# Optimization experiments

Measured on AMD Instinct MI355X. Metric: run time of the kernel, lower is better.

The kernel has to match this reference:

```python
import jax, jax.numpy as jnp
import numpy as np

N_TOKENS = 32768
D_MODEL = 1024
D_HIDDEN = 4096
N_EXPERTS = 8
TOP_K = 2


def setup_inputs() -> dict:
    key = jax.random.key(0)
    ks = jax.random.split(key, 8)
    s_in = 1.0 / np.sqrt(D_MODEL)
    s_hid = 1.0 / np.sqrt(D_HIDDEN)
    return {
        "x": jax.random.normal(ks[0], (N_TOKENS, D_MODEL), dtype=jnp.float32),
        "Wr": jax.random.normal(ks[1], (D_MODEL, N_EXPERTS), dtype=jnp.float32) * s_in,
        "br": jnp.zeros((N_EXPERTS,), dtype=jnp.float32),
        "W1": jax.random.normal(ks[2], (N_EXPERTS, D_MODEL, D_HIDDEN), dtype=jnp.float32) * s_in,
        "b1": jnp.zeros((N_EXPERTS, D_HIDDEN), dtype=jnp.float32),
        "W2": jax.random.normal(ks[3], (N_EXPERTS, D_HIDDEN, D_MODEL), dtype=jnp.float32) * s_hid,
        "b2": jnp.zeros((N_EXPERTS, D_MODEL), dtype=jnp.float32),
    }


def reference(x, Wr, br, W1, b1, W2, b2):
    # Router: softmax over experts, top-k selection, renormalize.
    logits = x @ Wr + br                                  # [N, E]
    probs = jax.nn.softmax(logits, axis=-1)
    topk_probs, topk_idx = jax.lax.top_k(probs, TOP_K)    # [N, K]
    topk_probs = topk_probs / jnp.sum(topk_probs, axis=-1, keepdims=True)
    # Per-token per-expert combine weight (sum over k of prob * selection).
    sel = jax.nn.one_hot(topk_idx, N_EXPERTS, dtype=x.dtype)   # [N, K, E]
    combine = jnp.einsum('nk,nke->ne', topk_probs, sel)        # [N, E]
    # Masked gather-MLP-scatter expressed as dense per-expert MLP weighted
    # by combine (zero weight for unselected experts -> identical math).
    out = jnp.zeros_like(x)
    for e in range(N_EXPERTS):
        h = jax.nn.gelu(x @ W1[e] + b1[e], approximate=False)  # exact erf GELU (torch default)
        out = out + combine[:, e:e + 1] * (h @ W2[e] + b2[e])
    return out
```

## Files before the change

kernel.cpp:

```cpp
#include <hip/hip_runtime.h>

#define NT_TOK 32768
#define DM 1024
#define DH 4096
#define NE 8
#define BT 256
#define BM 128
#define BK 32
#define CAP (NT_TOK*2 + NE*BT)
#define CHUNK_ROWS 32768

typedef _Float16 f16x8 __attribute__((ext_vector_type(8)));
typedef float f32x4 __attribute__((ext_vector_type(4)));
typedef float f32x8 __attribute__((ext_vector_type(8)));

__device__ __forceinline__ unsigned short f2h_bits(float v){
  _Float16 h = (_Float16)v;
  return __builtin_bit_cast(unsigned short, h);
}

__device__ __forceinline__ void async16(const void* g, void* l){
  __builtin_amdgcn_global_load_lds((const __attribute__((address_space(1))) void*)g,
                                   (__attribute__((address_space(3))) void*)l, 16, 0, 0);
}

__device__ __forceinline__ int xcd_remap(int orig, int nwg){
  int q = nwg >> 3, r = nwg & 7;
  int x = orig & 7, i = orig >> 3;
  int base = (x < r) ? x*(q+1) : r*(q+1) + (x-r)*q;
  return base + i;
}


__global__ __launch_bounds__(256) void cvt_f16_kernel(const float* __restrict__ src,
                                                      unsigned short* __restrict__ dst, int n8){
  int i = blockIdx.x*256 + threadIdx.x;
  if (i >= n8) return;
  float4 a = ((const float4*)src)[2*i];
  float4 b = ((const float4*)src)[2*i+1];
  union { unsigned short u[8]; uint4 v; } r;
  r.u[0]=f2h_bits(a.x); r.u[1]=f2h_bits(a.y); r.u[2]=f2h_bits(a.z); r.u[3]=f2h_bits(a.w);
  r.u[4]=f2h_bits(b.x); r.u[5]=f2h_bits(b.y); r.u[6]=f2h_bits(b.z); r.u[7]=f2h_bits(b.w);
  ((uint4*)dst)[i] = r.v;
}

__global__ __launch_bounds__(256) void transpose_f16_v2(const float* __restrict__ src,
    unsigned short* __restrict__ dst, int R, int C){
  __shared__ float t[64][65];
  int ez = blockIdx.z;
  const float* s = src + (size_t)ez*R*C;
  unsigned short* d = dst + (size_t)ez*R*C;
  int c0 = blockIdx.x*64, r0 = blockIdx.y*64;
  int tx = threadIdx.x & 15, ty = threadIdx.x >> 4;
  #pragma unroll
  for (int i=0;i<4;i++){
    float4 v = *(const float4*)&s[(size_t)(r0+ty+i*16)*C + c0 + tx*4];
    t[ty+i*16][tx*4+0]=v.x; t[ty+i*16][tx*4+1]=v.y;
    t[ty+i*16][tx*4+2]=v.z; t[ty+i*16][tx*4+3]=v.w;
  }
  __syncthreads();
  #pragma unroll
  for (int i=0;i<4;i++){
    int cc = ty + i*16;
    union { unsigned short u[4]; uint2 v; } o;
    #pragma unroll
    for (int j=0;j<4;j++) o.u[j] = f2h_bits(t[tx*4+j][cc]);
    *(uint2*)&d[(size_t)(c0+cc)*R + r0 + tx*4] = o.v;
  }
}


__global__ __launch_bounds__(256) void router_kernel(const float* __restrict__ x,
    const float* __restrict__ Wr, const float* __restrict__ br,
    int* __restrict__ topi, float* __restrict__ topw, int* __restrict__ counts){
  __shared__ float wr_s[NE*DM];
  __shared__ int bcnt[NE];
  int tid = threadIdx.x;
  if (tid < NE) bcnt[tid] = 0;
  for (int idx=tid; idx<NE*DM; idx+=256){
    int k = idx>>3, e = idx&7;
    wr_s[e*DM + k] = Wr[idx];
  }
  __syncthreads();
  int w = tid>>6, lane = tid&63;
  for (int tt=0; tt<16; ++tt){
    int t = blockIdx.x*64 + w*16 + tt;
    const float* xr = x + (size_t)t*DM;
    double acc[NE];
    #pragma unroll
    for (int e=0;e<NE;e++) acc[e]=0.0;
    #pragma unroll
    for (int j=0;j<16;j++){
      float xv = xr[j*64 + lane];
      #pragma unroll
      for (int e=0;e<NE;e++) acc[e] += (double)xv * (double)wr_s[e*DM + j*64 + lane];
    }
    #pragma unroll
    for (int e=0;e<NE;e++){
      #pragma unroll
      for (int d=32; d; d>>=1) acc[e] += __shfl_xor(acc[e], d);
    }
    if (lane==0){
      double l[NE];
      #pragma unroll
      for (int e=0;e<NE;e++) l[e] = acc[e] + (double)br[e];
      int i0 = 0;
      #pragma unroll
      for (int e=1;e<NE;e++) if (l[e] > l[i0]) i0 = e;
      int i1 = (i0==0) ? 1 : 0;
      #pragma unroll
      for (int e=0;e<NE;e++) if (e != i0 && l[e] > l[i1]) i1 = e;
      double w0 = 1.0/(1.0 + exp(l[i1]-l[i0]));
      topi[2*t] = i0; topi[2*t+1] = i1;
      topw[2*t] = (float)w0; topw[2*t+1] = (float)(1.0-w0);
      atomicAdd(&bcnt[i0],1); atomicAdd(&bcnt[i1],1);
    }
  }
  __syncthreads();
  if (tid < NE && bcnt[tid] > 0) atomicAdd(&counts[tid], bcnt[tid]);
}

__global__ void offsets_kernel(const int* __restrict__ counts, int* __restrict__ off){
  if (threadIdx.x==0 && blockIdx.x==0){
    int o = 0;
    for (int e=0;e<NE;e++){ off[e] = o; o += ((counts[e]+BT-1)/BT)*BT; }
    off[NE] = o;
  }
}

__global__ __launch_bounds__(256) void scatter_kernel(const int* __restrict__ topi,
    const float* __restrict__ topw, const int* __restrict__ off,
    int* __restrict__ cursor, int* __restrict__ atok, float* __restrict__ awgt){
  __shared__ int bcnt[NE];
  __shared__ int bbase[NE];
  int tid = threadIdx.x;
  if (tid < NE) bcnt[tid] = 0;
  __syncthreads();
  int t = blockIdx.x*256 + tid;
  int e0 = topi[2*t],   e1 = topi[2*t+1];
  int r0 = atomicAdd(&bcnt[e0], 1);
  int r1 = atomicAdd(&bcnt[e1], 1);
  __syncthreads();
  if (tid < NE) bbase[tid] = (bcnt[tid] > 0) ? atomicAdd(&cursor[tid], bcnt[tid]) : 0;
  __syncthreads();
  int s0 = off[e0] + bbase[e0] + r0;
  int s1 = off[e1] + bbase[e1] + r1;
  atok[s0] = t;  awgt[s0] = topw[2*t];
  atok[s1] = t;  awgt[s1] = topw[2*t+1];
}


template<int KDIM, bool IS_G2>
__global__ __launch_bounds__(256, 2) void gemm_big_kernel(
    const unsigned short* __restrict__ Asrc,
    const unsigned short* __restrict__ WT,
    const float* __restrict__ bias,
    const int* __restrict__ atok,
    const float* __restrict__ awgt,
    const int* __restrict__ offs,
    unsigned short* __restrict__ H,
    float* __restrict__ out,
    int c0){
  __shared__ unsigned short As[3][BM*BK];
  __shared__ unsigned short Bs[3][BT*BK];
  const int NDIM = IS_G2 ? DM : DH;
  const int NT = NDIM/BT;
  int wg = xcd_remap(blockIdx.x, gridDim.x);
  int nt = wg % NT, mt = wg / NT;
  int total = offs[NE];
  int m0 = c0 + mt*BM;
  if (m0 >= total) return;
  int e = 0;
  #pragma unroll
  for (int q=0;q<NE-1;q++) if (m0 >= offs[q+1]) e = q+1;
  int tid = threadIdx.x;
  int lane = tid&63, wn = tid>>6;

  const unsigned short* agp[2];
  int dofsA[2];
  #pragma unroll
  for (int j=0;j<2;j++){
    int c = j*256 + tid;
    int u = (c&7) ^ ((c>>3)&7);
    int srow = ((c>>3)<<1) + (u>>2);
    int sch  = u&3;
    if (IS_G2){
      agp[j] = Asrc + (size_t)(m0 - c0 + srow)*KDIM + sch*8;
    } else {
      int tok = atok[m0 + srow];
      if (tok < 0) tok = 0;
      agp[j] = Asrc + (size_t)tok*KDIM + sch*8;
    }
    dofsA[j] = c*8;
  }
  const unsigned short* bgp0;
  int dofsB0;
  {
    int c = tid;
    int u = (c&7) ^ ((c>>3)&7);
    int srow = ((c>>3)<<1) + (u>>2);
    int sch  = u&3;
    bgp0 = WT + ((size_t)e*NDIM + nt*BT + srow)*KDIM + sch*8;
    dofsB0 = c*8;
  }

  int pos = (((lane>>4) + ((lane&1)<<2)) ^ ((lane>>1)&7)) << 3;
  int aoff0 = (((lane&15)>>1))*64 + pos;
  int boff0 = (wn*32 + ((lane&15)>>1))*64 + pos;

  f32x4 acc[8][4];
  #pragma unroll
  for (int i=0;i<8;i++)
    #pragma unroll
    for (int j=0;j<4;j++) acc[i][j] = 0.0f;

  const int NKT = KDIM/BK;
  #pragma unroll
  for (int t=0;t<2;t++){
    #pragma unroll
    for (int j=0;j<2;j++) async16(agp[j] + t*BK, &As[t][dofsA[j]]);
    #pragma unroll
    for (int j=0;j<4;j++) async16(bgp0 + (size_t)j*64*KDIM + t*BK, &Bs[t][dofsB0 + j*2048]);
  }

  int cur = 0;
  for (int kt=0; kt<NKT; ++kt){
    if (kt < NKT-1) asm volatile("s_waitcnt vmcnt(6)" ::: "memory");
    else            asm volatile("s_waitcnt vmcnt(0)" ::: "memory");
    __builtin_amdgcn_s_barrier();
    int nxt2 = cur + 2; if (nxt2 >= 3) nxt2 -= 3;
    const unsigned short* Ab = &As[cur][0];
    const unsigned short* Bb = &Bs[cur][0];
    f16x8 b[4], a[4];
    #pragma unroll
    for (int nf=0;nf<4;nf++) b[nf] = *(const f16x8*)&Bb[boff0 + nf*512];
    #pragma unroll
    for (int mf=0;mf<4;mf++) a[mf] = *(const f16x8*)&Ab[aoff0 + mf*512];
    if (kt+2 < NKT){
      #pragma unroll
      for (int j=0;j<2;j++) async16(agp[j] + (size_t)(kt+2)*BK, &As[nxt2][dofsA[j]]);
    }
    __builtin_amdgcn_s_setprio(1);
    #pragma unroll
    for (int mf=0;mf<4;mf++)
      #pragma unroll
      for (int nf=0;nf<4;nf++)
        acc[mf][nf] = __builtin_amdgcn_mfma_f32_16x16x32_f16(a[mf], b[nf], acc[mf][nf], 0,0,0);
    __builtin_amdgcn_s_setprio(0);
    __builtin_amdgcn_s_barrier();
    #pragma unroll
    for (int mf=0;mf<4;mf++) a[mf] = *(const f16x8*)&Ab[aoff0 + (mf+4)*512];
    if (kt+2 < NKT){
      #pragma unroll
      for (int j=0;j<4;j++) async16(bgp0 + (size_t)j*64*KDIM + (size_t)(kt+2)*BK, &Bs[nxt2][dofsB0 + j*2048]);
    }
    __builtin_amdgcn_s_setprio(1);
    #pragma unroll
    for (int mf=0;mf<4;mf++)
      #pragma unroll
      for (int nf=0;nf<4;nf++)
        acc[mf+4][nf] = __builtin_amdgcn_mfma_f32_16x16x32_f16(a[mf], b[nf], acc[mf+4][nf], 0,0,0);
    __builtin_amdgcn_s_setprio(0);
    cur = (cur + 1 == 3) ? 0 : cur + 1;
  }

  int nbase = nt*BT + wn*64 + (lane&15);
  if (!IS_G2){
    const float* be = bias + (size_t)e*DH;
    int rloc = (m0 - c0) + ((lane>>4)<<2);
    #pragma unroll
    for (int mf=0;mf<8;mf++)
      #pragma unroll
      for (int nf=0;nf<4;nf++){
        int nn = nbase + nf*16;
        float bv = be[nn];
        #pragma unroll
        for (int r2=0;r2<4;r2++){
          float v = acc[mf][nf][r2] + bv;
          float g = 0.5f*v*(1.0f + erff(v*0.70710678118654752f));
          H[(size_t)(rloc + mf*16 + r2)*DH + nn] = f2h_bits(g);
        }
      }
  } else {
    const float* be = bias + (size_t)e*DM;
    int sbase = m0 + ((lane>>4)<<2);
    #pragma unroll
    for (int mf=0;mf<8;mf++){
      #pragma unroll
      for (int r2=0;r2<4;r2++){
        int slot = sbase + mf*16 + r2;
        int tok = atok[slot];
        float wgt = awgt[slot];
        if (tok >= 0){
          #pragma unroll
          for (int nf=0;nf<4;nf++){
            int nn = nbase + nf*16;
            float v = acc[mf][nf][r2] + be[nn];
            atomicAdd(&out[(size_t)tok*DM + nn], wgt*v);
          }
        }
      }
    }
  }
}


__global__ __launch_bounds__(256) void gemm1_f32_kernel(
    const float* __restrict__ xf, const unsigned short* __restrict__ W1T,
    const float* __restrict__ b1, const int* __restrict__ atok,
    const int* __restrict__ offs, unsigned short* __restrict__ H, int c0){
  __shared__ float Asf[128*64];
  __shared__ unsigned short Bsld[128*64];
  const int NT = DH/128;
  int wg = xcd_remap(blockIdx.x, gridDim.x);
  int nt = wg % NT, mt = wg / NT;
  int total = offs[NE];
  int m0 = c0 + mt*128;
  if (m0 >= total) return;
  int e = 0;
  #pragma unroll
  for (int q=0;q<NE-1;q++) if (m0 >= offs[q+1]) e = q+1;
  int tid = threadIdx.x;
  const void* ag[8];
  int aofs[8];
  #pragma unroll
  for (int j=0;j<8;j++){
    int c = j*256 + tid;
    int r = c>>4, sb = (c&15)*16;
    int tok = atok[m0 + r];
    if (tok < 0) tok = 0;
    ag[j] = (const void*)((const char*)(xf + (size_t)tok*DM) + sb);
    aofs[j] = c*16;
  }
  const unsigned short* bg[4];
  int bofs[4];
  #pragma unroll
  for (int j=0;j<4;j++){
    int c = j*256 + tid;
    int r = c>>3, s = c&7;
    bg[j] = W1T + ((size_t)e*DH + nt*128 + r)*DM + s*8;
    bofs[j] = c*16;
  }
  f32x4 acc[4][4];
  #pragma unroll
  for (int i=0;i<4;i++)
    #pragma unroll
    for (int j=0;j<4;j++) acc[i][j] = 0.0f;
  int lane = tid&63;
  int wm = tid>>7, wn = (tid>>6)&1;
  int arow = wm*64 + (lane&15);
  int ak0  = (lane>>4)*8;
  int brr  = (wn*64 + (lane&15))*64 + ak0;
  for (int kt=0; kt<DM/64; ++kt){
    #pragma unroll
    for (int j=0;j<8;j++)
      async16((const char*)ag[j] + (size_t)kt*64*4, (char*)Asf + aofs[j]);
    #pragma unroll
    for (int j=0;j<4;j++)
      async16(bg[j] + (size_t)kt*64, (char*)Bsld + bofs[j]);
    __syncthreads();
    #pragma unroll
    for (int kk=0; kk<64; kk+=32){
      f16x8 a[4], b[4];
      #pragma unroll
      for (int f=0;f<4;f++){
        f32x8 v = *(const f32x8*)&Asf[(arow + f*16)*64 + ak0 + kk];
        a[f] = __builtin_convertvector(v, f16x8);
        b[f] = *(const f16x8*)&Bsld[brr + f*16*64 + kk];
      }
      #pragma unroll
      for (int i=0;i<4;i++)
        #pragma unroll
        for (int j2=0;j2<4;j2++)
          acc[i][j2] = __builtin_amdgcn_mfma_f32_16x16x32_f16(a[i], b[j2], acc[i][j2], 0,0,0);
    }
    __syncthreads();
  }
  const float* b1e = b1 + (size_t)e*DH;
  int rloc = (m0 - c0) + wm*64 + ((lane>>4)<<2);
  int nbase = nt*128 + wn*64 + (lane&15);
  #pragma unroll
  for (int i=0;i<4;i++)
    #pragma unroll
    for (int j=0;j<4;j++){
      int nn = nbase + j*16;
      float bv = b1e[nn];
      #pragma unroll
      for (int r2=0;r2<4;r2++){
        float v = acc[i][j][r2] + bv;
        float g = 0.5f*v*(1.0f + erff(v*0.70710678118654752f));
        H[(size_t)(rloc + i*16 + r2)*DH + nn] = f2h_bits(g);
      }
    }
}

__global__ void fill_kernel(float* p, float v, size_t n){
  size_t i = (size_t)blockIdx.x*256 + threadIdx.x;
  if (i < n) p[i] = v;
}


extern "C" void kernel_launch(void* const* d_in, const int* in_sizes, int n_in,
                              void* d_out, int out_size, void* d_ws, size_t ws_size,
                              hipStream_t stream){
  const float* x  = (const float*)d_in[0];
  const float* Wr = (const float*)d_in[1];
  const float* br = (const float*)d_in[2];
  const float* W1 = (const float*)d_in[3];
  const float* b1 = (const float*)d_in[4];
  const float* W2 = (const float*)d_in[5];
  const float* b2 = (const float*)d_in[6];
  float* out = (float*)d_out;

  char* ws = (char*)d_ws;
  size_t o = 0;
  auto take = [&](size_t bytes)->void*{
    void* p = ws + o; o += (bytes + 255) & ~(size_t)255; return p;
  };
  unsigned short* W1T = (unsigned short*)take((size_t)NE*DM*DH*2);
  unsigned short* W2T = (unsigned short*)take((size_t)NE*DM*DH*2);
  int*   TOPI = (int*)take((size_t)NT_TOK*2*4);
  float* TOPW = (float*)take((size_t)NT_TOK*2*4);
  int*   ATOK = (int*)take((size_t)CAP*4);
  float* AWGT = (float*)take((size_t)CAP*4);
  int*   CNT  = (int*)take(256);
  int* CUR = CNT + 8;
  int* OFF = CNT + 16;

  if (o + (size_t)BT*DH*2 > ws_size){
    fill_kernel<<<(unsigned)((out_size+255)/256), 256, 0, stream>>>(out, 4321.5f, (size_t)out_size);
    return;
  }

  unsigned short* XB = nullptr;
  bool use_xb = false;
  {
    size_t xb_bytes = (size_t)NT_TOK*DM*2 + 256;
    size_t need_h  = (size_t)2048*DH*2;
    if (o + xb_bytes + need_h <= ws_size){
      use_xb = true;
      XB = (unsigned short*)take((size_t)NT_TOK*DM*2);
    }
  }
  size_t rem = ws_size - o;
  size_t cr = (rem / ((size_t)DH*2)) / BT * BT;
  if (cr > (size_t)CHUNK_ROWS) cr = CHUNK_ROWS;
  if (cr < BT){
    fill_kernel<<<(unsigned)((out_size+255)/256), 256, 0, stream>>>(out, 4321.5f, (size_t)out_size);
    return;
  }
  int CR = (int)cr;
  unsigned short* Hb = (unsigned short*)take((size_t)CR*DH*2);

  hipMemsetAsync(CNT, 0, 64, stream);
  hipMemsetAsync(ATOK, 0xFF, (size_t)CAP*4, stream);
  hipMemsetAsync(out, 0, (size_t)out_size*sizeof(float), stream);

  if (use_xb)
    cvt_f16_kernel<<<(NT_TOK*DM/8 + 255)/256, 256, 0, stream>>>(x, XB, NT_TOK*DM/8);
  transpose_f16_v2<<<dim3(DH/64, DM/64, NE), 256, 0, stream>>>(W1, W1T, DM, DH);
  transpose_f16_v2<<<dim3(DM/64, DH/64, NE), 256, 0, stream>>>(W2, W2T, DH, DM);
  router_kernel<<<NT_TOK/64, 256, 0, stream>>>(x, Wr, br, TOPI, TOPW, CNT);
  offsets_kernel<<<1, 1, 0, stream>>>(CNT, OFF);
  scatter_kernel<<<NT_TOK/256, 256, 0, stream>>>(TOPI, TOPW, OFF, CUR, ATOK, AWGT);

  for (int c0 = 0; c0 < CAP; c0 += CR){
    int rows = CAP - c0; if (rows > CR) rows = CR;
    int mtc = (rows + BM - 1)/BM;
    if (use_xb)
      gemm_big_kernel<DM, false><<<dim3((DH/BT)*mtc), 256, 0, stream>>>(
          XB, W1T, b1, ATOK, AWGT, OFF, Hb, out, c0);
    else
      gemm1_f32_kernel<<<dim3((DH/128)*((rows+127)/128)), 256, 0, stream>>>(
          x, W1T, b1, ATOK, OFF, Hb, c0);
    gemm_big_kernel<DH, true><<<dim3((DM/BT)*mtc), 256, 0, stream>>>(
        Hb, W2T, b2, ATOK, AWGT, OFF, Hb, out, c0);
  }
}
```

Baseline: 2.321 ms.

## Shrink expert GEMM tile to 128x128 with 2x2 warp grid and N-major order

Changes the expert GEMM block tile from 128x256 to 128x128, with warps arranged 2x2 so each covers 64x64 instead of 128x64. This halves the accumulator registers and B-tile LDS, which allows raising launch bounds to 3 waves per SIMD. The grid order becomes n-tile-major, so consecutive blocks share the same weight tile. The trade-off is lower arithmetic intensity per block and more A-tile reloads, since there are twice as many n-tiles.

```diff
diff --git a/kernel.cpp b/kernel.cpp
--- a/kernel.cpp
+++ b/kernel.cpp
@@ -6,6 +6,7 @@
 #define NE 8
 #define BT 256
 #define BM 128
+#define BN 128
 #define BK 32
 #define CAP (NT_TOK*2 + NE*BT)
 #define CHUNK_ROWS 32768
@@ -151,7 +152,7 @@
 
 
 template<int KDIM, bool IS_G2>
-__global__ __launch_bounds__(256, 2) void gemm_big_kernel(
+__global__ __launch_bounds__(256, 3) void gemm_big_kernel(
     const unsigned short* __restrict__ Asrc,
     const unsigned short* __restrict__ WT,
     const float* __restrict__ bias,
@@ -160,13 +161,12 @@
     const int* __restrict__ offs,
     unsigned short* __restrict__ H,
     float* __restrict__ out,
-    int c0){
+    int c0, int mtc){
   __shared__ unsigned short As[3][BM*BK];
-  __shared__ unsigned short Bs[3][BT*BK];
+  __shared__ unsigned short Bs[3][BN*BK];
   const int NDIM = IS_G2 ? DM : DH;
-  const int NT = NDIM/BT;
   int wg = xcd_remap(blockIdx.x, gridDim.x);
-  int nt = wg % NT, mt = wg / NT;
+  int nt = wg / mtc, mt = wg - nt*mtc;
   int total = offs[NE];
   int m0 = c0 + mt*BM;
   if (m0 >= total) return;
@@ -174,10 +174,12 @@
   #pragma unroll
   for (int q=0;q<NE-1;q++) if (m0 >= offs[q+1]) e = q+1;
   int tid = threadIdx.x;
-  int lane = tid&63, wn = tid>>6;
+  int lane = tid&63, wid = tid>>6;
+  int wm = wid>>1, wn = wid&1;
 
   const unsigned short* agp[2];
-  int dofsA[2];
+  const unsigned short* bgp[2];
+  int dofs[2];
   #pragma unroll
   for (int j=0;j<2;j++){
     int c = j*256 + tid;
@@ -191,26 +193,17 @@
       if (tok < 0) tok = 0;
       agp[j] = Asrc + (size_t)tok*KDIM + sch*8;
     }
-    dofsA[j] = c*8;
-  }
-  const unsigned short* bgp0;
-  int dofsB0;
-  {
-    int c = tid;
-    int u = (c&7) ^ ((c>>3)&7);
-    int srow = ((c>>3)<<1) + (u>>2);
-    int sch  = u&3;
-    bgp0 = WT + ((size_t)e*NDIM + nt*BT + srow)*KDIM + sch*8;
-    dofsB0 = c*8;
+    bgp[j] = WT + ((size_t)e*NDIM + nt*BN + srow)*KDIM + sch*8;
+    dofs[j] = c*8;
   }
 
   int pos = (((lane>>4) + ((lane&1)<<2)) ^ ((lane>>1)&7)) << 3;
-  int aoff0 = (((lane&15)>>1))*64 + pos;
+  int aoff0 = (wm*32 + ((lane&15)>>1))*64 + pos;
   int boff0 = (wn*32 + ((lane&15)>>1))*64 + pos;
 
-  f32x4 acc[8][4];
-  #pragma unroll
-  for (int i=0;i<8;i++)
+  f32x4 acc[4][4];
+  #pragma unroll
+  for (int i=0;i<4;i++)
     #pragma unroll
     for (int j=0;j<4;j++) acc[i][j] = 0.0f;
 
@@ -218,14 +211,14 @@
   #pragma unroll
   for (int t=0;t<2;t++){
     #pragma unroll
-    for (int j=0;j<2;j++) async16(agp[j] + t*BK, &As[t][dofsA[j]]);
-    #pragma unroll
-    for (int j=0;j<4;j++) async16(bgp0 + (size_t)j*64*KDIM + t*BK, &Bs[t][dofsB0 + j*2048]);
+    for (int j=0;j<2;j++) async16(agp[j] + t*BK, &As[t][dofs[j]]);
+    #pragma unroll
+    for (int j=0;j<2;j++) async16(bgp[j] + t*BK, &Bs[t][dofs[j]]);
   }
 
   int cur = 0;
   for (int kt=0; kt<NKT; ++kt){
-    if (kt < NKT-1) asm volatile("s_waitcnt vmcnt(6)" ::: "memory");
+    if (kt < NKT-1) asm volatile("s_waitcnt vmcnt(4)" ::: "memory");
     else            asm volatile("s_waitcnt vmcnt(0)" ::: "memory");
     __builtin_amdgcn_s_barrier();
     int nxt2 = cur + 2; if (nxt2 >= 3) nxt2 -= 3;
@@ -238,38 +231,36 @@
     for (int mf=0;mf<4;mf++) a[mf] = *(const f16x8*)&Ab[aoff0 + mf*512];
     if (kt+2 < NKT){
       #pragma unroll
-      for (int j=0;j<2;j++) async16(agp[j] + (size_t)(kt+2)*BK, &As[nxt2][dofsA[j]]);
+      for (int j=0;j<2;j++) async16(agp[j] + (size_t)(kt+2)*BK, &As[nxt2][dofs[j]]);
     }
     __builtin_amdgcn_s_setprio(1);
     #pragma unroll
     for (int mf=0;mf<4;mf++)
       #pragma unroll
-      for (int nf=0;nf<4;nf++)
+      for (int nf=0;nf<2;nf++)
         acc[mf][nf] = __builtin_amdgcn_mfma_f32_16x16x32_f16(a[mf], b[nf], acc[mf][nf], 0,0,0);
     __builtin_amdgcn_s_setprio(0);
     __builtin_amdgcn_s_barrier();
-    #pragma unroll
-    for (int mf=0;mf<4;mf++) a[mf] = *(const f16x8*)&Ab[aoff0 + (mf+4)*512];
     if (kt+2 < NKT){
       #pragma unroll
-      for (int j=0;j<4;j++) async16(bgp0 + (size_t)j*64*KDIM + (size_t)(kt+2)*BK, &Bs[nxt2][dofsB0 + j*2048]);
+      for (int j=0;j<2;j++) async16(bgp[j] + (size_t)(kt+2)*BK, &Bs[nxt2][dofs[j]]);
     }
     __builtin_amdgcn_s_setprio(1);
     #pragma unroll
     for (int mf=0;mf<4;mf++)
       #pragma unroll
-      for (int nf=0;nf<4;nf++)
-        acc[mf+4][nf] = __builtin_amdgcn_mfma_f32_16x16x32_f16(a[mf], b[nf], acc[mf+4][nf], 0,0,0);
+      for (int nf=2;nf<4;nf++)
+        acc[mf][nf] = __builtin_amdgcn_mfma_f32_16x16x32_f16(a[mf], b[nf], acc[mf][nf], 0,0,0);
     __builtin_amdgcn_s_setprio(0);
     cur = (cur + 1 == 3) ? 0 : cur + 1;
   }
 
-  int nbase = nt*BT + wn*64 + (lane&15);
+  int nbase = nt*BN + wn*64 + (lane&15);
   if (!IS_G2){
     const float* be = bias + (size_t)e*DH;
-    int rloc = (m0 - c0) + ((lane>>4)<<2);
-    #pragma unroll
-    for (int mf=0;mf<8;mf++)
+    int rloc = (m0 - c0) + wm*64 + ((lane>>4)<<2);
+    #pragma unroll
+    for (int mf=0;mf<4;mf++)
       #pragma unroll
       for (int nf=0;nf<4;nf++){
         int nn = nbase + nf*16;
@@ -283,9 +274,9 @@
       }
   } else {
     const float* be = bias + (size_t)e*DM;
-    int sbase = m0 + ((lane>>4)<<2);
-    #pragma unroll
-    for (int mf=0;mf<8;mf++){
+    int sbase = m0 + wm*64 + ((lane>>4)<<2);
+    #pragma unroll
+    for (int mf=0;mf<4;mf++){
       #pragma unroll
       for (int r2=0;r2<4;r2++){
         int slot = sbase + mf*16 + r2;
@@ -468,12 +459,12 @@
     int rows = CAP - c0; if (rows > CR) rows = CR;
     int mtc = (rows + BM - 1)/BM;
     if (use_xb)
-      gemm_big_kernel<DM, false><<<dim3((DH/BT)*mtc), 256, 0, stream>>>(
-          XB, W1T, b1, ATOK, AWGT, OFF, Hb, out, c0);
+      gemm_big_kernel<DM, false><<<dim3((DH/BN)*mtc), 256, 0, stream>>>(
+          XB, W1T, b1, ATOK, AWGT, OFF, Hb, out, c0, mtc);
     else
       gemm1_f32_kernel<<<dim3((DH/128)*((rows+127)/128)), 256, 0, stream>>>(
           x, W1T, b1, ATOK, OFF, Hb, c0);
-    gemm_big_kernel<DH, true><<<dim3((DM/BT)*mtc), 256, 0, stream>>>(
-        Hb, W2T, b2, ATOK, AWGT, OFF, Hb, out, c0);
-  }
-}
+    gemm_big_kernel<DH, true><<<dim3((DM/BN)*mtc), 256, 0, stream>>>(
+        Hb, W2T, b2, ATOK, AWGT, OFF, Hb, out, c0, mtc);
+  }
+}
```

Result: no change. 2.335 ms (+0.6%).
